# Optimization experiments

Hardware: AMD Instinct MI355X
Metric: run time of the kernel (lower is better)

Reference implementation:

```python
import jax, jax.numpy as jnp
import numpy as np

B, IC, H, W = 4, 512, 128, 128
INTER = IC // 32  # 16
C3 = 3 * INTER    # 48
EPS = 1e-5


def conv(x, w, b, pad, groups=1):
    y = jax.lax.conv_general_dilated(
        x, w, window_strides=(1, 1), padding=pad,
        dimension_numbers=('NCHW', 'OIHW', 'NCHW'),
        feature_group_count=groups)
    return y + b[None, :, None, None]


def bn(x, g, b, m, v):
    scale = (g * jax.lax.rsqrt(v + EPS))[None, :, None, None]
    return (x - m[None, :, None, None]) * scale + b[None, :, None, None]


def erode(x):
    # cv2.erode with ones(3,3): 3x3 sliding-window min, borders neutral (+inf)
    return jax.lax.reduce_window(x, jnp.array(jnp.inf, x.dtype), jax.lax.min,
                                 (1, 1, 3, 3), (1, 1, 1, 1), 'SAME')


def dilate(x):
    # cv2.dilate with ones(3,3): 3x3 sliding-window max, borders neutral (-inf)
    return jax.lax.reduce_window(x, jnp.array(-jnp.inf, x.dtype), jax.lax.max,
                                 (1, 1, 3, 3), (1, 1, 1, 1), 'SAME')


PH = [(1, 1), (0, 0)]  # (3,1)/(5,1) use vertical padding variants
PV = [(0, 0), (1, 1)]
PH5 = [(2, 2), (0, 0)]
PV5 = [(0, 0), (2, 2)]
P33 = [(1, 1), (1, 1)]


def gated_attention_fwd(ex, dx,
                        Dw1, Db1, Dw31, Db31, Dw13, Db13, Dw51, Db51, Dw15, Db15,
                        Dg, Dbe, Dm, Dv,
                        Ew1, Eb1, Ew31, Eb31, Ew13, Eb13, Ew51, Eb51, Ew15, Eb15,
                        Eg, Ebe, Em, Ev,
                        dww, dwb, pww, pwb,
                        qw, qb, kw, kb, vw, vb, rw, rb, cw, cb):
    b, c, h, w = ex.shape
    # ---- StripedConv subnetwork on dx ----
    dilX = dilate(dx)
    eroX = erode(dx)
    Dx1 = conv(dilX, Dw1, Db1, 'VALID')
    Dx31 = conv(dilX, Dw31, Db31, PH)
    Dx3113 = conv(Dx31, Dw13, Db13, PV)
    Dx51 = conv(dilX, Dw51, Db51, PH5)
    Dx5115 = conv(Dx51, Dw15, Db15, PV5)
    Ex1 = conv(eroX, Ew1, Eb1, 'VALID')
    Ex31 = conv(eroX, Ew31, Eb31, PH)
    Ex3113 = conv(Ex31, Ew13, Eb13, PV)
    Ex51 = conv(eroX, Ew51, Eb51, PH5)
    Ex5115 = conv(Ex51, Ew15, Eb15, PV5)
    difference = Dx1 - Ex51 + Dx1 - Ex31 + Dx31 - Ex1 + Dx51 - Ex1  # [b,16,h,w]
    dilF = jax.nn.relu(bn(jnp.concatenate([Dx1, Dx3113, Dx5115], axis=1), Dg, Dbe, Dm, Dv))
    eroF = jax.nn.relu(bn(jnp.concatenate([Ex1, Ex3113, Ex5115], axis=1), Eg, Ebe, Em, Ev))
    edge = jax.nn.relu(conv(conv(dilF - eroF, dww, dwb, P33, groups=C3), pww, pwb, 'VALID'))
    # ---- Gated attention on ex ----
    Q = conv(ex, qw, qb, 'VALID').reshape(b, INTER, -1)          # [b,16,hw]
    K = conv(ex, kw, kb, 'VALID').reshape(b, -1, INTER)          # reshape (NOT transpose), faithful to torch .view
    Wedge = jax.nn.sigmoid(conv(
        jnp.concatenate([jnp.mean(edge, axis=1, keepdims=True),
                         jnp.max(edge, axis=1, keepdims=True)], axis=1),
        cw, cb, 'VALID'))                                        # [b,1,h,w]
    V = conv(ex, vw, vb, 'VALID')
    V = (V * Wedge + V).reshape(b, INTER, -1)                    # [b,16,hw]
    diff = difference.reshape(b, -1, INTER)                      # [b,hw,16] via reshape
    weight = jnp.matmul(Q, K)                                    # [b,16,16]
    gate = jnp.matmul(Q, diff)                                   # [b,16,16]
    weights = jax.nn.softmax(weight + gate, axis=1)              # softmax over dim=1, per original
    atten = jnp.matmul(weights, V)                               # [b,16,hw]
    attenX = jnp.transpose(atten, (0, 2, 1)).reshape(b, INTER, h, w)
    out = conv(attenX, rw, rb, 'VALID') + dx                     # [b,512,h,w]
    return out


def setup_inputs() -> dict:
    key = jax.random.key(0)
    ks = iter(jax.random.split(key, 80))
    def rn(shape, s=0.05):
        return jax.random.normal(next(ks), shape, jnp.float32) * s
    inp = {}
    inp['ex'] = jax.random.normal(next(ks), (B, IC, H, W), jnp.float32)
    inp['dx'] = jax.random.normal(next(ks), (B, IC, H, W), jnp.float32)
    for p in ('D', 'E'):
        inp[p + 'w1'] = rn((INTER, IC, 1, 1)); inp[p + 'b1'] = rn((INTER,))
        inp[p + 'w31'] = rn((INTER, IC, 3, 1)); inp[p + 'b31'] = rn((INTER,))
        inp[p + 'w13'] = rn((INTER, INTER, 1, 3)); inp[p + 'b13'] = rn((INTER,))
        inp[p + 'w51'] = rn((INTER, IC, 5, 1)); inp[p + 'b51'] = rn((INTER,))
        inp[p + 'w15'] = rn((INTER, INTER, 1, 5)); inp[p + 'b15'] = rn((INTER,))
        inp[p + 'g'] = 1.0 + rn((C3,)); inp[p + 'be'] = rn((C3,))
        inp[p + 'm'] = rn((C3,), 0.1)
        inp[p + 'v'] = jax.random.uniform(next(ks), (C3,), jnp.float32, 0.5, 1.5)
    inp['dww'] = rn((C3, 1, 3, 3)); inp['dwb'] = rn((C3,))
    inp['pww'] = rn((INTER, C3, 1, 1)); inp['pwb'] = rn((INTER,))
    inp['qw'] = rn((INTER, IC, 1, 1)); inp['qb'] = rn((INTER,))
    inp['kw'] = rn((INTER, IC, 1, 1)); inp['kb'] = rn((INTER,))
    inp['vw'] = rn((INTER, IC, 1, 1)); inp['vb'] = rn((INTER,))
    inp['rw'] = rn((IC, INTER, 1, 1)); inp['rb'] = rn((IC,))
    inp['cw'] = rn((1, 2, 1, 1)); inp['cb'] = rn((1,))
    return inp


def reference(ex, dx,
              Dw1, Db1, Dw31, Db31, Dw13, Db13, Dw51, Db51, Dw15, Db15,
              Dg, Dbe, Dm, Dv,
              Ew1, Eb1, Ew31, Eb31, Ew13, Eb13, Ew51, Eb51, Ew15, Eb15,
              Eg, Ebe, Em, Ev,
              dww, dwb, pww, pwb,
              qw, qb, kw, kb, vw, vb, rw, rb, cw, cb):
    return gated_attention_fwd(ex, dx,
                               Dw1, Db1, Dw31, Db31, Dw13, Db13, Dw51, Db51, Dw15, Db15,
                               Dg, Dbe, Dm, Dv,
                               Ew1, Eb1, Ew31, Eb31, Ew13, Eb13, Ew51, Eb51, Ew15, Eb15,
                               Eg, Ebe, Em, Ev,
                               dww, dwb, pww, pwb,
                               qw, qb, kw, kb, vw, vb, rw, rb, cw, cb)
```

## Files before the change

### kernel.cpp

```cpp
#include <hip/hip_runtime.h>
#include <hip/hip_bf16.h>

typedef __hip_bfloat16 bf16_t;
typedef __attribute__((ext_vector_type(8))) short short8;
typedef __attribute__((ext_vector_type(4))) float floatx4;

constexpr int N_  = 4;
constexpr int C_  = 512;
constexpr int H_  = 128;
constexpr int W_  = 128;
constexpr int HW_ = H_ * W_;
constexpr int O144 = 144;
constexpr int C3_ = 48;

constexpr size_t OFF_DILT = 0;
constexpr size_t OFF_EROT = 67108864;
constexpr size_t OFF_PD   = 134217728;
constexpr size_t OFF_PE   = 171966464;
constexpr size_t OFF_WD   = 209715200;
constexpr size_t OFF_WE   = 210010112;
constexpr size_t OFF_WQ   = 210305024;
constexpr size_t OFF_BQ   = 210403328;
constexpr size_t OFF_WSUM = 210403584;
constexpr size_t OFF_WSM  = 210407680;
constexpr size_t OFF_DX1   = 0;
constexpr size_t OFF_DX31  = 4194304;
constexpr size_t OFF_DX51  = 8388608;
constexpr size_t OFF_EX1   = 12582912;
constexpr size_t OFF_EX31  = 16777216;
constexpr size_t OFF_EX51  = 20971520;
constexpr size_t OFF_DIFF  = 25165824;
constexpr size_t OFF_F     = 29360128;
constexpr size_t OFF_QKV   = 41943040;
constexpr size_t OFF_AX    = 54525952;
constexpr size_t OFF_WEDGE = 58720256;
constexpr size_t OFF_E16   = 67108864;

__global__ void prep_weights(const float* __restrict__ Dw1, const float* __restrict__ Dw31,
                             const float* __restrict__ Dw51,
                             const float* __restrict__ Ew1, const float* __restrict__ Ew31,
                             const float* __restrict__ Ew51,
                             const float* __restrict__ qw, const float* __restrict__ kw,
                             const float* __restrict__ vw,
                             const float* __restrict__ qb, const float* __restrict__ kb,
                             const float* __restrict__ vb,
                             bf16_t* __restrict__ WD, bf16_t* __restrict__ WE,
                             float* __restrict__ WQ, float* __restrict__ BQ) {
  int idx = blockIdx.x * 256 + threadIdx.x;
  const int sz = O144 * C_;
  if (idx < sz) {
    int r = idx / C_, c = idx % C_;
    float v;
    if (r < 16)       v = Dw1[r * C_ + c];
    else if (r < 64)  { int t = (r - 16) >> 4, o = (r - 16) & 15; v = Dw31[(o * C_ + c) * 3 + t]; }
    else              { int t = (r - 64) >> 4, o = (r - 64) & 15; v = Dw51[(o * C_ + c) * 5 + t]; }
    WD[idx] = __float2bfloat16(v);
    if (r < 16)       v = Ew1[r * C_ + c];
    else if (r < 64)  { int t = (r - 16) >> 4, o = (r - 16) & 15; v = Ew31[(o * C_ + c) * 3 + t]; }
    else              { int t = (r - 64) >> 4, o = (r - 64) & 15; v = Ew51[(o * C_ + c) * 5 + t]; }
    WE[idx] = __float2bfloat16(v);
  } else if (idx < sz + C3_ * C_) {
    int k = idx - sz;
    int r = k / C_, c = k % C_;
    const float* w = (r < 16) ? qw : (r < 32) ? kw : vw;
    WQ[k] = w[(r & 15) * C_ + c];
  } else if (idx < sz + C3_ * C_ + C3_) {
    int r = idx - sz - C3_ * C_;
    const float* bb = (r < 16) ? qb : (r < 32) ? kb : vb;
    BQ[r] = bb[r & 15];
  }
}

__device__ __forceinline__ void accrow(const float* __restrict__ rowp, int ax, int x0, int dx4,
                                       float* vmax, float* vmin) {
  float buf[16];
  *(float4*)&buf[0]  = *(const float4*)(rowp + ax);
  *(float4*)&buf[4]  = *(const float4*)(rowp + x0);
  *(float4*)&buf[8]  = *(const float4*)(rowp + x0 + 4);
  *(float4*)&buf[12] = *(const float4*)(rowp + dx4);
  #pragma unroll
  for (int j = 0; j < 10; ++j) {
    vmax[j] = fmaxf(vmax[j], buf[j + 3]);
    vmin[j] = fminf(vmin[j], buf[j + 3]);
  }
}

__global__ __launch_bounds__(256) void dilero_t(const float* __restrict__ dxin,
                                                bf16_t* __restrict__ dilT,
                                                bf16_t* __restrict__ eroT) {
  int cT = blockIdx.x, y = blockIdx.y, b = blockIdx.z;
  int t = threadIdx.x;
  int cl = t >> 4;
  int xg = t & 15, x0 = xg * 8;
  int c = cT * 16 + cl;
  const float* p = dxin + ((size_t)(b * C_ + c)) * HW_;
  int ax  = (x0 == 0)   ? 0   : x0 - 4;
  int dx4 = (x0 == 120) ? 124 : x0 + 8;
  float vmax[10], vmin[10];
  #pragma unroll
  for (int j = 0; j < 10; ++j) { vmax[j] = -INFINITY; vmin[j] = INFINITY; }
  if (y > 0)   accrow(p + (y - 1) * W_, ax, x0, dx4, vmax, vmin);
  accrow(p + y * W_, ax, x0, dx4, vmax, vmin);
  if (y < 127) accrow(p + (y + 1) * W_, ax, x0, dx4, vmax, vmin);
  if (xg == 0)  { vmax[0] = -INFINITY; vmin[0] = INFINITY; }
  if (xg == 15) { vmax[9] = -INFINITY; vmin[9] = INFINITY; }
  __shared__ bf16_t ds_d[128][18];
  __shared__ bf16_t ds_e[128][18];
  #pragma unroll
  for (int i = 0; i < 8; ++i) {
    float mx = fmaxf(fmaxf(vmax[i], vmax[i + 1]), vmax[i + 2]);
    float mn = fminf(fminf(vmin[i], vmin[i + 1]), vmin[i + 2]);
    ds_d[x0 + i][cl] = __float2bfloat16(mx);
    ds_e[x0 + i][cl] = __float2bfloat16(mn);
  }
  __syncthreads();
  int j = t & 127;
  const uint* rp = (t >> 7) ? (const uint*)&ds_e[j][0] : (const uint*)&ds_d[j][0];
  uint v0 = rp[0], v1 = rp[1], v2 = rp[2], v3 = rp[3];
  uint v4 = rp[4], v5 = rp[5], v6 = rp[6], v7 = rp[7];
  bf16_t* dst = (t >> 7) ? eroT : dilT;
  size_t base = ((size_t)(b * HW_ + y * W_ + j)) * C_ + cT * 16;
  uint4* op = (uint4*)(dst + base);
  op[0] = make_uint4(v0, v1, v2, v3);
  op[1] = make_uint4(v4, v5, v6, v7);
}

__global__ __launch_bounds__(256) void gemm_mfma(const bf16_t* __restrict__ WDb,
                                                 const bf16_t* __restrict__ WEb,
                                                 const bf16_t* __restrict__ DILt,
                                                 const bf16_t* __restrict__ EROt,
                                                 float* __restrict__ PD,
                                                 float* __restrict__ PE) {
  constexpr int LDA = 40;
  constexpr int LDB = 40;
  __shared__ bf16_t As[48 * LDA];
  __shared__ bf16_t Bs[128 * LDB];
  int z = blockIdx.z;
  int b = z & 3, map = z >> 2;
  const bf16_t* Wb = map ? WEb : WDb;
  const bf16_t* Xt = map ? EROt : DILt;
  float* Out = map ? PE : PD;
  int m0 = blockIdx.y * 48;
  int p0 = blockIdx.x * 128;
  int tid = threadIdx.x;
  int wave = tid >> 6, lane = tid & 63;
  int quad = lane >> 4, l16 = lane & 15;
  floatx4 acc[3][2] = {};
  const bf16_t* Xb = Xt + ((size_t)b * HW_ + p0) * C_;
  for (int k0 = 0; k0 < C_; k0 += 32) {
    if (tid < 192) {
      int m = tid >> 2, q = tid & 3;
      uint4 v = *(const uint4*)(Wb + (size_t)(m0 + m) * C_ + k0 + q * 8);
      *(uint4*)(&As[m * LDA + q * 8]) = v;
    }
    #pragma unroll
    for (int s = 0; s < 2; ++s) {
      int slot = tid + s * 256;
      int pp = slot >> 2, q = slot & 3;
      uint4 v = *(const uint4*)(Xb + (size_t)pp * C_ + k0 + q * 8);
      *(uint4*)(&Bs[pp * LDB + q * 8]) = v;
    }
    __syncthreads();
    short8 bfr[2];
    #pragma unroll
    for (int nt = 0; nt < 2; ++nt)
      bfr[nt] = *(const short8*)(&Bs[(wave * 32 + nt * 16 + l16) * LDB + quad * 8]);
    #pragma unroll
    for (int mt = 0; mt < 3; ++mt) {
      short8 afr = *(const short8*)(&As[(mt * 16 + l16) * LDA + quad * 8]);
      #pragma unroll
      for (int nt = 0; nt < 2; ++nt)
        acc[mt][nt] = __builtin_amdgcn_mfma_f32_16x16x32_bf16(afr, bfr[nt], acc[mt][nt], 0, 0, 0);
    }
    __syncthreads();
  }
  #pragma unroll
  for (int mt = 0; mt < 3; ++mt)
    #pragma unroll
    for (int nt = 0; nt < 2; ++nt) {
      int n = p0 + wave * 32 + nt * 16 + l16;
      #pragma unroll
      for (int r = 0; r < 4; ++r) {
        int m = m0 + mt * 16 + quad * 4 + r;
        Out[((size_t)b * O144 + m) * HW_ + n] = acc[mt][nt][r];
      }
    }
}

__global__ __launch_bounds__(256) void gemm48f(const float* __restrict__ X,
                                               const float* __restrict__ Wm,
                                               const float* __restrict__ bias,
                                               float* __restrict__ Out) {
  int b  = blockIdx.z;
  int p0 = blockIdx.x * 128;
  __shared__ __align__(16) float Xs[16][128];
  __shared__ __align__(16) float Ws[16][8][8];
  int tid = threadIdx.x;
  int pg  = tid & 31;
  int og  = tid >> 5;
  float acc[6][4] = {};
  const float* Xb = X + (size_t)b * C_ * HW_;
  for (int k0 = 0; k0 < C_; k0 += 16) {
    {
      int e = tid * 8;
      int kk = e >> 7, px = e & 127;
      float4 a = *(const float4*)(Xb + (size_t)(k0 + kk) * HW_ + p0 + px);
      float4 bv = *(const float4*)(Xb + (size_t)(k0 + kk) * HW_ + p0 + px + 4);
      *(float4*)&Xs[kk][px] = a;
      *(float4*)&Xs[kk][px + 4] = bv;
    }
    #pragma unroll
    for (int i = 0; i < 3; ++i) {
      int e = tid * 3 + i;
      int oo = e >> 4, kk = e & 15;
      Ws[kk][oo / 6][oo % 6] = Wm[(size_t)oo * C_ + k0 + kk];
    }
    __syncthreads();
    #pragma unroll
    for (int kk = 0; kk < 16; ++kk) {
      float4 xv = *(const float4*)&Xs[kk][pg * 4];
      float4 wa = *(const float4*)&Ws[kk][og][0];
      float2 wb = *(const float2*)&Ws[kk][og][4];
      float wv[6] = {wa.x, wa.y, wa.z, wa.w, wb.x, wb.y};
      float xs[4] = {xv.x, xv.y, xv.z, xv.w};
      #pragma unroll
      for (int o = 0; o < 6; ++o)
        #pragma unroll
        for (int pq = 0; pq < 4; ++pq) acc[o][pq] += wv[o] * xs[pq];
    }
    __syncthreads();
  }
  #pragma unroll
  for (int o = 0; o < 6; ++o) {
    int oc = og * 6 + o;
    float bi = bias[oc];
    float4 r;
    r.x = acc[o][0] + bi; r.y = acc[o][1] + bi; r.z = acc[o][2] + bi; r.w = acc[o][3] + bi;
    *(float4*)&Out[((size_t)b * C3_ + oc) * HW_ + p0 + pg * 4] = r;
  }
}

__global__ void combine(const float* __restrict__ PD, const float* __restrict__ PE,
                        const float* __restrict__ Db1, const float* __restrict__ Db31,
                        const float* __restrict__ Db51,
                        const float* __restrict__ Eb1, const float* __restrict__ Eb31,
                        const float* __restrict__ Eb51,
                        float* __restrict__ Dx1, float* __restrict__ Dx31, float* __restrict__ Dx51,
                        float* __restrict__ Ex1, float* __restrict__ Ex31, float* __restrict__ Ex51,
                        float* __restrict__ Diff) {
  int idx = blockIdx.x * 256 + threadIdx.x;
  int pix = idx & (HW_ - 1);
  int o = (idx >> 14) & 15;
  int b = idx >> 18;
  int y = pix >> 7;
  const float* pd = PD + (size_t)b * O144 * HW_;
  const float* pe = PE + (size_t)b * O144 * HW_;
  float d1 = pd[o * HW_ + pix] + Db1[o];
  float e1 = pe[o * HW_ + pix] + Eb1[o];
  float d31 = Db31[o], e31 = Eb31[o];
  #pragma unroll
  for (int t = 0; t < 3; ++t) {
    int yy = y - 1 + t;
    if (yy >= 0 && yy < H_) {
      int pp = pix + (t - 1) * W_;
      d31 += pd[(16 + t * 16 + o) * HW_ + pp];
      e31 += pe[(16 + t * 16 + o) * HW_ + pp];
    }
  }
  float d51 = Db51[o], e51 = Eb51[o];
  #pragma unroll
  for (int t = 0; t < 5; ++t) {
    int yy = y - 2 + t;
    if (yy >= 0 && yy < H_) {
      int pp = pix + (t - 2) * W_;
      d51 += pd[(64 + t * 16 + o) * HW_ + pp];
      e51 += pe[(64 + t * 16 + o) * HW_ + pp];
    }
  }
  Dx1[idx] = d1;  Ex1[idx] = e1;
  Dx31[idx] = d31; Ex31[idx] = e31;
  Dx51[idx] = d51; Ex51[idx] = e51;
  Diff[idx] = 2.f * d1 + d31 + d51 - 2.f * e1 - e31 - e51;
}

__device__ __forceinline__ void loadwin(const float* __restrict__ rowp, int xb, float* buf) {
  int a0 = (xb == 0)   ? 0   : xb - 4;
  int c0 = (xb == 124) ? 124 : xb + 4;
  *(float4*)&buf[0] = *(const float4*)(rowp + a0);
  *(float4*)&buf[4] = *(const float4*)(rowp + xb);
  *(float4*)&buf[8] = *(const float4*)(rowp + c0);
  if (xb == 0)   { buf[0] = buf[1] = buf[2] = buf[3] = 0.f; }
  if (xb == 124) { buf[8] = buf[9] = buf[10] = buf[11] = 0.f; }
}

__global__ __launch_bounds__(256) void fkern(const float* __restrict__ Dx1, const float* __restrict__ Dx31,
                      const float* __restrict__ Dx51,
                      const float* __restrict__ Ex1, const float* __restrict__ Ex31,
                      const float* __restrict__ Ex51,
                      const float* __restrict__ Dw13, const float* __restrict__ Db13,
                      const float* __restrict__ Dw15, const float* __restrict__ Db15,
                      const float* __restrict__ Ew13, const float* __restrict__ Eb13,
                      const float* __restrict__ Ew15, const float* __restrict__ Eb15,
                      const float* __restrict__ Dg, const float* __restrict__ Dbe,
                      const float* __restrict__ Dm, const float* __restrict__ Dv,
                      const float* __restrict__ Eg, const float* __restrict__ Ebe,
                      const float* __restrict__ Em, const float* __restrict__ Ev,
                      float* __restrict__ F) {
  int idx = blockIdx.x * 256 + threadIdx.x;
  int xq = idx & 4095;
  int ch = (idx >> 12) % 48;
  int b  = (idx >> 12) / 48;
  int pix4 = xq * 4;
  int xb = (xq & 31) * 4;
  int rowoff = pix4 - xb;
  float dval[4], eval[4];
  if (ch < 16) {
    const float* dp = Dx1 + (((size_t)(b * 16 + ch)) << 14) + pix4;
    const float* ep = Ex1 + (((size_t)(b * 16 + ch)) << 14) + pix4;
    float4 dv = *(const float4*)dp, ev = *(const float4*)ep;
    dval[0]=dv.x; dval[1]=dv.y; dval[2]=dv.z; dval[3]=dv.w;
    eval[0]=ev.x; eval[1]=ev.y; eval[2]=ev.z; eval[3]=ev.w;
  } else if (ch < 32) {
    int o = ch - 16;
    float da[4] = {Db13[o], Db13[o], Db13[o], Db13[o]};
    float ea[4] = {Eb13[o], Eb13[o], Eb13[o], Eb13[o]};
    for (int m = 0; m < 16; ++m) {
      float bd[12], be[12];
      loadwin(Dx31 + (((size_t)(b * 16 + m)) << 14) + rowoff, xb, bd);
      loadwin(Ex31 + (((size_t)(b * 16 + m)) << 14) + rowoff, xb, be);
      #pragma unroll
      for (int t = 0; t < 3; ++t) {
        float wd = Dw13[(o * 16 + m) * 3 + t];
        float we = Ew13[(o * 16 + m) * 3 + t];
        #pragma unroll
        for (int i = 0; i < 4; ++i) {
          da[i] += wd * bd[i + t + 3];
          ea[i] += we * be[i + t + 3];
        }
      }
    }
    #pragma unroll
    for (int i = 0; i < 4; ++i) { dval[i] = da[i]; eval[i] = ea[i]; }
  } else {
    int o = ch - 32;
    float da[4] = {Db15[o], Db15[o], Db15[o], Db15[o]};
    float ea[4] = {Eb15[o], Eb15[o], Eb15[o], Eb15[o]};
    for (int m = 0; m < 16; ++m) {
      float bd[12], be[12];
      loadwin(Dx51 + (((size_t)(b * 16 + m)) << 14) + rowoff, xb, bd);
      loadwin(Ex51 + (((size_t)(b * 16 + m)) << 14) + rowoff, xb, be);
      #pragma unroll
      for (int t = 0; t < 5; ++t) {
        float wd = Dw15[(o * 16 + m) * 5 + t];
        float we = Ew15[(o * 16 + m) * 5 + t];
        #pragma unroll
        for (int i = 0; i < 4; ++i) {
          da[i] += wd * bd[i + t + 2];
          ea[i] += we * be[i + t + 2];
        }
      }
    }
    #pragma unroll
    for (int i = 0; i < 4; ++i) { dval[i] = da[i]; eval[i] = ea[i]; }
  }
  float sD = Dg[ch] * rsqrtf(Dv[ch] + 1e-5f);
  float sE = Eg[ch] * rsqrtf(Ev[ch] + 1e-5f);
  float4 r;
  float* rr = (float*)&r;
  #pragma unroll
  for (int i = 0; i < 4; ++i) {
    float fD = fmaxf((dval[i] - Dm[ch]) * sD + Dbe[ch], 0.f);
    float fE = fmaxf((eval[i] - Em[ch]) * sE + Ebe[ch], 0.f);
    rr[i] = fD - fE;
  }
  *(float4*)&F[(((size_t)(b * 48 + ch)) << 14) + pix4] = r;
}

__global__ __launch_bounds__(256) void edgeA(const float* __restrict__ F, const float* __restrict__ dww,
                      const float* __restrict__ dwb, const float* __restrict__ pww,
                      const float* __restrict__ pwb, float* __restrict__ E16) {
  int idx = blockIdx.x * 256 + threadIdx.x;
  int xq = idx & 4095;
  int o  = (idx >> 12) & 15;
  int b  = idx >> 16;
  int pix4 = xq * 4;
  int xb = (xq & 31) * 4;
  int y  = pix4 >> 7;
  int rowoff = pix4 - xb - y * W_;
  const float* Fb = F + (((size_t)b * 48) << 14);
  float e[4] = {pwb[o], pwb[o], pwb[o], pwb[o]};
  for (int g = 0; g < 48; ++g) {
    float dw[4] = {dwb[g], dwb[g], dwb[g], dwb[g]};
    const float* plane = Fb + ((size_t)g << 14);
    #pragma unroll
    for (int dy = 0; dy < 3; ++dy) {
      int yy = y - 1 + dy;
      if (yy < 0 || yy >= H_) continue;
      float buf[12];
      loadwin(plane + yy * W_ + rowoff, xb, buf);
      #pragma unroll
      for (int t = 0; t < 3; ++t) {
        float w = dww[g * 9 + dy * 3 + t];
        #pragma unroll
        for (int i = 0; i < 4; ++i) dw[i] += w * buf[i + t + 3];
      }
    }
    float pw = pww[o * 48 + g];
    #pragma unroll
    for (int i = 0; i < 4; ++i) e[i] += pw * dw[i];
  }
  float4 r;
  r.x = fmaxf(e[0], 0.f); r.y = fmaxf(e[1], 0.f);
  r.z = fmaxf(e[2], 0.f); r.w = fmaxf(e[3], 0.f);
  *(float4*)&E16[(((size_t)(b * 16 + o)) << 14) + pix4] = r;
}

__global__ void edgeB(const float* __restrict__ E16, const float* __restrict__ cw,
                      const float* __restrict__ cb, float* __restrict__ Wedge) {
  int idx = blockIdx.x * 256 + threadIdx.x;
  int pix = idx & (HW_ - 1);
  int b = idx >> 14;
  float sum = 0.f, mx = -INFINITY;
  #pragma unroll
  for (int o = 0; o < 16; ++o) {
    float v = E16[(((size_t)(b * 16 + o)) << 14) + pix];
    sum += v; mx = fmaxf(mx, v);
  }
  float z = cw[0] * (sum * (1.f / 16.f)) + cw[1] * mx + cb[0];
  Wedge[idx] = 1.f / (1.f + expf(-z));
}

__global__ void attn_qk(const float* __restrict__ QKV, const float* __restrict__ Diff,
                        float* __restrict__ wsum) {
  int b = blockIdx.y;
  int i = threadIdx.x >> 4, j = threadIdx.x & 15;
  const float* Q  = QKV + (size_t)b * C3_ * HW_;
  const float* Kf = Q + 16 * HW_;
  const float* Df = Diff + (size_t)b * 16 * HW_;
  __shared__ float Qs[16][512];
  __shared__ float KD[512][16];
  float acc = 0.f;
  int p0 = blockIdx.x * 2048;
  for (int c0 = p0; c0 < p0 + 2048; c0 += 512) {
    for (int e = threadIdx.x; e < 16 * 512; e += 256) {
      int r = e >> 9, p = e & 511;
      Qs[r][p] = Q[(r << 14) + c0 + p];
    }
    for (int e = threadIdx.x; e < 512 * 16; e += 256) {
      int f = (c0 << 4) + e;
      KD[e >> 4][e & 15] = Kf[f] + Df[f];
    }
    __syncthreads();
    for (int p = 0; p < 512; ++p) acc += Qs[i][p] * KD[p][j];
    __syncthreads();
  }
  atomicAdd(&wsum[(b << 8) + threadIdx.x], acc);
}

__global__ void softmaxk(const float* __restrict__ wsum, float* __restrict__ wsm) {
  int b = blockIdx.x;
  __shared__ float s[16][16];
  __shared__ float colmx[16], colsum[16];
  int i = threadIdx.x >> 4, j = threadIdx.x & 15;
  s[i][j] = wsum[(b << 8) + threadIdx.x];
  __syncthreads();
  if (threadIdx.x < 16) {
    int jj = threadIdx.x;
    float mx = -INFINITY;
    for (int ii = 0; ii < 16; ++ii) mx = fmaxf(mx, s[ii][jj]);
    float sm = 0.f;
    for (int ii = 0; ii < 16; ++ii) sm += expf(s[ii][jj] - mx);
    colmx[jj] = mx; colsum[jj] = sm;
  }
  __syncthreads();
  wsm[(b << 8) + threadIdx.x] = expf(s[i][j] - colmx[j]) / colsum[j];
}

__global__ void attenx_k(const float* __restrict__ QKV, const float* __restrict__ wsm,
                         const float* __restrict__ Wedge, float* __restrict__ AX) {
  int idx = blockIdx.x * 256 + threadIdx.x;
  int pix = idx & (HW_ - 1);
  int m = (idx >> 14) & 15;
  int b = idx >> 18;
  __shared__ float ws[256];
  ws[threadIdx.x] = wsm[(b << 8) + threadIdx.x];
  __syncthreads();
  int q = (m << 10) + (pix >> 4);
  int r = pix & 15;
  const float* V = QKV + (size_t)b * C3_ * HW_ + (size_t)32 * HW_;
  float a = 0.f;
  #pragma unroll
  for (int s = 0; s < 16; ++s) a += ws[(r << 4) + s] * V[(s << 14) + q];
  AX[idx] = a * (1.f + Wedge[(b << 14) + q]);
}

__global__ __launch_bounds__(256) void finalconv(const float* __restrict__ AX,
                                                 const float* __restrict__ rw,
                                                 const float* __restrict__ rb,
                                                 const float* __restrict__ dxin,
                                                 float* __restrict__ out) {
  int blk = blockIdx.x;
  int b = blk >> 6;
  int p0 = (blk & 63) << 8;
  __shared__ float ax[16][256];
  for (int e = threadIdx.x; e < 16 * 256; e += 256) {
    int m = e >> 8, p = e & 255;
    ax[m][p] = AX[((size_t)(b * 16 + m) << 14) + p0 + p];
  }
  __syncthreads();
  int p = threadIdx.x;
  for (int oc = 0; oc < 512; ++oc) {
    float a = rb[oc];
    #pragma unroll
    for (int m = 0; m < 16; ++m) a += rw[oc * 16 + m] * ax[m][p];
    size_t oi = ((size_t)(b * C_ + oc) << 14) + p0 + p;
    out[oi] = a + dxin[oi];
  }
}

extern "C" void kernel_launch(void* const* d_in, const int* in_sizes, int n_in,
                              void* d_out, int out_size, void* d_ws, size_t ws_size,
                              hipStream_t stream) {
  (void)in_sizes; (void)n_in; (void)out_size; (void)ws_size;
  const float* ex   = (const float*)d_in[0];
  const float* dx   = (const float*)d_in[1];
  const float* Dw1  = (const float*)d_in[2];
  const float* Db1  = (const float*)d_in[3];
  const float* Dw31 = (const float*)d_in[4];
  const float* Db31 = (const float*)d_in[5];
  const float* Dw13 = (const float*)d_in[6];
  const float* Db13 = (const float*)d_in[7];
  const float* Dw51 = (const float*)d_in[8];
  const float* Db51 = (const float*)d_in[9];
  const float* Dw15 = (const float*)d_in[10];
  const float* Db15 = (const float*)d_in[11];
  const float* Dg   = (const float*)d_in[12];
  const float* Dbe  = (const float*)d_in[13];
  const float* Dm   = (const float*)d_in[14];
  const float* Dv   = (const float*)d_in[15];
  const float* Ew1  = (const float*)d_in[16];
  const float* Eb1  = (const float*)d_in[17];
  const float* Ew31 = (const float*)d_in[18];
  const float* Eb31 = (const float*)d_in[19];
  const float* Ew13 = (const float*)d_in[20];
  const float* Eb13 = (const float*)d_in[21];
  const float* Ew51 = (const float*)d_in[22];
  const float* Eb51 = (const float*)d_in[23];
  const float* Ew15 = (const float*)d_in[24];
  const float* Eb15 = (const float*)d_in[25];
  const float* Eg   = (const float*)d_in[26];
  const float* Ebe  = (const float*)d_in[27];
  const float* Em   = (const float*)d_in[28];
  const float* Ev   = (const float*)d_in[29];
  const float* dww  = (const float*)d_in[30];
  const float* dwb  = (const float*)d_in[31];
  const float* pww  = (const float*)d_in[32];
  const float* pwb  = (const float*)d_in[33];
  const float* qw   = (const float*)d_in[34];
  const float* qb   = (const float*)d_in[35];
  const float* kw   = (const float*)d_in[36];
  const float* kb   = (const float*)d_in[37];
  const float* vw   = (const float*)d_in[38];
  const float* vb   = (const float*)d_in[39];
  const float* rw   = (const float*)d_in[40];
  const float* rb   = (const float*)d_in[41];
  const float* cw   = (const float*)d_in[42];
  const float* cb   = (const float*)d_in[43];

  char* ws = (char*)d_ws;
  bf16_t* DILt = (bf16_t*)(ws + OFF_DILT);
  bf16_t* EROt = (bf16_t*)(ws + OFF_EROT);
  float* PD   = (float*)(ws + OFF_PD);
  float* PE   = (float*)(ws + OFF_PE);
  bf16_t* WDb = (bf16_t*)(ws + OFF_WD);
  bf16_t* WEb = (bf16_t*)(ws + OFF_WE);
  float* WQ   = (float*)(ws + OFF_WQ);
  float* BQ   = (float*)(ws + OFF_BQ);
  float* WSUM = (float*)(ws + OFF_WSUM);
  float* WSM  = (float*)(ws + OFF_WSM);
  float* DX1  = (float*)(ws + OFF_DX1);
  float* DX31 = (float*)(ws + OFF_DX31);
  float* DX51 = (float*)(ws + OFF_DX51);
  float* EX1  = (float*)(ws + OFF_EX1);
  float* EX31 = (float*)(ws + OFF_EX31);
  float* EX51 = (float*)(ws + OFF_EX51);
  float* DIFF = (float*)(ws + OFF_DIFF);
  float* Fb   = (float*)(ws + OFF_F);
  float* QKV  = (float*)(ws + OFF_QKV);
  float* AX   = (float*)(ws + OFF_AX);
  float* WEDG = (float*)(ws + OFF_WEDGE);
  float* E16  = (float*)(ws + OFF_E16);

  prep_weights<<<385, 256, 0, stream>>>(Dw1, Dw31, Dw51, Ew1, Ew31, Ew51,
                                        qw, kw, vw, qb, kb, vb, WDb, WEb, WQ, BQ);
  dilero_t<<<dim3(32, 128, 4), 256, 0, stream>>>(dx, DILt, EROt);
  gemm_mfma<<<dim3(128, 3, 8), 256, 0, stream>>>(WDb, WEb, DILt, EROt, PD, PE);
  combine<<<(N_ * 16 * HW_) / 256, 256, 0, stream>>>(PD, PE, Db1, Db31, Db51, Eb1, Eb31, Eb51,
                                                     DX1, DX31, DX51, EX1, EX31, EX51, DIFF);
  gemm48f<<<dim3(HW_ / 128, 1, N_), 256, 0, stream>>>(ex, WQ, BQ, QKV);
  fkern<<<(N_ * 48 * (HW_ / 4)) / 256, 256, 0, stream>>>(DX1, DX31, DX51, EX1, EX31, EX51,
                                                   Dw13, Db13, Dw15, Db15, Ew13, Eb13, Ew15, Eb15,
                                                   Dg, Dbe, Dm, Dv, Eg, Ebe, Em, Ev, Fb);
  edgeA<<<(N_ * 16 * (HW_ / 4)) / 256, 256, 0, stream>>>(Fb, dww, dwb, pww, pwb, E16);
  edgeB<<<(N_ * HW_) / 256, 256, 0, stream>>>(E16, cw, cb, WEDG);
  hipMemsetAsync(ws + OFF_WSUM, 0, 4096, stream);
  attn_qk<<<dim3(8, N_), 256, 0, stream>>>(QKV, DIFF, WSUM);
  softmaxk<<<N_, 256, 0, stream>>>(WSUM, WSM);
  attenx_k<<<(N_ * 16 * HW_) / 256, 256, 0, stream>>>(QKV, WSM, WEDG, AX);
  finalconv<<<(N_ * HW_) / 256, 256, 0, stream>>>(AX, rw, rb, dx, (float*)d_out);
}
```

Measured before the change: 919.7 us.

## Widen MFMA GEMM M-tile, split edge depthwise/pointwise, vectorize final conv

The bf16 MFMA GEMM now computes all 144 output rows per block instead of splitting them into three 48-row tiles, so each activation tile is loaded once rather than three times. The edge branch, which used to redo the 48-channel depthwise conv for each of 16 outputs, now runs the depthwise conv once into a buffer and a second kernel applies the pointwise conv, ReLU and gating. The final 1x1 conv uses float4 loads and stores, with each thread covering 32 output channels. The costs are more accumulator registers in the GEMM (lower occupancy, fewer blocks), an extra 48-channel intermediate buffer, and a 48-entry register array in edgeB2.

```diff
diff --git a/kernel.cpp b/kernel.cpp
--- a/kernel.cpp
+++ b/kernel.cpp
@@ -34,7 +34,7 @@
 constexpr size_t OFF_QKV   = 41943040;
 constexpr size_t OFF_AX    = 54525952;
 constexpr size_t OFF_WEDGE = 58720256;
-constexpr size_t OFF_E16   = 67108864;
+constexpr size_t OFF_DW    = 67108864;
 
 __global__ void prep_weights(const float* __restrict__ Dw1, const float* __restrict__ Dw31,
                              const float* __restrict__ Dw51,
@@ -133,32 +133,36 @@
                                                  float* __restrict__ PE) {
   constexpr int LDA = 40;
   constexpr int LDB = 40;
-  __shared__ bf16_t As[48 * LDA];
+  __shared__ bf16_t As[O144 * LDA];
   __shared__ bf16_t Bs[128 * LDB];
-  int z = blockIdx.z;
+  int z = blockIdx.y;
   int b = z & 3, map = z >> 2;
   const bf16_t* Wb = map ? WEb : WDb;
   const bf16_t* Xt = map ? EROt : DILt;
   float* Out = map ? PE : PD;
-  int m0 = blockIdx.y * 48;
   int p0 = blockIdx.x * 128;
   int tid = threadIdx.x;
   int wave = tid >> 6, lane = tid & 63;
   int quad = lane >> 4, l16 = lane & 15;
-  floatx4 acc[3][2] = {};
+  floatx4 acc[9][2] = {};
   const bf16_t* Xb = Xt + ((size_t)b * HW_ + p0) * C_;
   for (int k0 = 0; k0 < C_; k0 += 32) {
-    if (tid < 192) {
-      int m = tid >> 2, q = tid & 3;
-      uint4 v = *(const uint4*)(Wb + (size_t)(m0 + m) * C_ + k0 + q * 8);
-      *(uint4*)(&As[m * LDA + q * 8]) = v;
+    #pragma unroll
+    for (int s = 0; s < 2; ++s) {
+      int slot = tid + s * 256;
+      int m = slot >> 2, q = slot & 3;
+      *(uint4*)(&As[m * LDA + q * 8]) = *(const uint4*)(Wb + (size_t)m * C_ + k0 + q * 8);
+    }
+    if (tid < 64) {
+      int slot = tid + 512;
+      int m = slot >> 2, q = slot & 3;
+      *(uint4*)(&As[m * LDA + q * 8]) = *(const uint4*)(Wb + (size_t)m * C_ + k0 + q * 8);
     }
     #pragma unroll
     for (int s = 0; s < 2; ++s) {
       int slot = tid + s * 256;
       int pp = slot >> 2, q = slot & 3;
-      uint4 v = *(const uint4*)(Xb + (size_t)pp * C_ + k0 + q * 8);
-      *(uint4*)(&Bs[pp * LDB + q * 8]) = v;
+      *(uint4*)(&Bs[pp * LDB + q * 8]) = *(const uint4*)(Xb + (size_t)pp * C_ + k0 + q * 8);
     }
     __syncthreads();
     short8 bfr[2];
@@ -166,7 +170,7 @@
     for (int nt = 0; nt < 2; ++nt)
       bfr[nt] = *(const short8*)(&Bs[(wave * 32 + nt * 16 + l16) * LDB + quad * 8]);
     #pragma unroll
-    for (int mt = 0; mt < 3; ++mt) {
+    for (int mt = 0; mt < 9; ++mt) {
       short8 afr = *(const short8*)(&As[(mt * 16 + l16) * LDA + quad * 8]);
       #pragma unroll
       for (int nt = 0; nt < 2; ++nt)
@@ -175,13 +179,13 @@
     __syncthreads();
   }
   #pragma unroll
-  for (int mt = 0; mt < 3; ++mt)
+  for (int mt = 0; mt < 9; ++mt)
     #pragma unroll
     for (int nt = 0; nt < 2; ++nt) {
       int n = p0 + wave * 32 + nt * 16 + l16;
       #pragma unroll
       for (int r = 0; r < 4; ++r) {
-        int m = m0 + mt * 16 + quad * 4 + r;
+        int m = mt * 16 + quad * 4 + r;
         Out[((size_t)b * O144 + m) * HW_ + n] = acc[mt][nt][r];
       }
     }
@@ -376,55 +380,58 @@
   *(float4*)&F[(((size_t)(b * 48 + ch)) << 14) + pix4] = r;
 }
 
-__global__ __launch_bounds__(256) void edgeA(const float* __restrict__ F, const float* __restrict__ dww,
-                      const float* __restrict__ dwb, const float* __restrict__ pww,
-                      const float* __restrict__ pwb, float* __restrict__ E16) {
+__global__ __launch_bounds__(256) void edgeDW(const float* __restrict__ F,
+                                              const float* __restrict__ dww,
+                                              const float* __restrict__ dwb,
+                                              float* __restrict__ DW) {
   int idx = blockIdx.x * 256 + threadIdx.x;
   int xq = idx & 4095;
-  int o  = (idx >> 12) & 15;
-  int b  = idx >> 16;
+  int ch = (idx >> 12) % 48;
+  int b  = (idx >> 12) / 48;
   int pix4 = xq * 4;
   int xb = (xq & 31) * 4;
   int y  = pix4 >> 7;
-  int rowoff = pix4 - xb - y * W_;
-  const float* Fb = F + (((size_t)b * 48) << 14);
-  float e[4] = {pwb[o], pwb[o], pwb[o], pwb[o]};
-  for (int g = 0; g < 48; ++g) {
-    float dw[4] = {dwb[g], dwb[g], dwb[g], dwb[g]};
-    const float* plane = Fb + ((size_t)g << 14);
-    #pragma unroll
-    for (int dy = 0; dy < 3; ++dy) {
-      int yy = y - 1 + dy;
-      if (yy < 0 || yy >= H_) continue;
-      float buf[12];
-      loadwin(plane + yy * W_ + rowoff, xb, buf);
+  const float* plane = F + (((size_t)(b * 48 + ch)) << 14);
+  float acc[4];
+  float bi = dwb[ch];
+  acc[0] = bi; acc[1] = bi; acc[2] = bi; acc[3] = bi;
+  #pragma unroll
+  for (int dy = 0; dy < 3; ++dy) {
+    int yy = y - 1 + dy;
+    if (yy < 0 || yy >= H_) continue;
+    float buf[12];
+    loadwin(plane + yy * W_, xb, buf);
+    #pragma unroll
+    for (int t = 0; t < 3; ++t) {
+      float w = dww[ch * 9 + dy * 3 + t];
       #pragma unroll
-      for (int t = 0; t < 3; ++t) {
-        float w = dww[g * 9 + dy * 3 + t];
-        #pragma unroll
-        for (int i = 0; i < 4; ++i) dw[i] += w * buf[i + t + 3];
-      }
-    }
-    float pw = pww[o * 48 + g];
-    #pragma unroll
-    for (int i = 0; i < 4; ++i) e[i] += pw * dw[i];
-  }
-  float4 r;
-  r.x = fmaxf(e[0], 0.f); r.y = fmaxf(e[1], 0.f);
-  r.z = fmaxf(e[2], 0.f); r.w = fmaxf(e[3], 0.f);
-  *(float4*)&E16[(((size_t)(b * 16 + o)) << 14) + pix4] = r;
-}
-
-__global__ void edgeB(const float* __restrict__ E16, const float* __restrict__ cw,
-                      const float* __restrict__ cb, float* __restrict__ Wedge) {
+      for (int i = 0; i < 4; ++i) acc[i] += w * buf[i + t + 3];
+    }
+  }
+  float4 r; r.x = acc[0]; r.y = acc[1]; r.z = acc[2]; r.w = acc[3];
+  *(float4*)&DW[(((size_t)(b * 48 + ch)) << 14) + pix4] = r;
+}
+
+__global__ __launch_bounds__(256) void edgeB2(const float* __restrict__ DW,
+                                              const float* __restrict__ pww,
+                                              const float* __restrict__ pwb,
+                                              const float* __restrict__ cw,
+                                              const float* __restrict__ cb,
+                                              float* __restrict__ Wedge) {
   int idx = blockIdx.x * 256 + threadIdx.x;
   int pix = idx & (HW_ - 1);
   int b = idx >> 14;
+  float dwv[48];
+  #pragma unroll
+  for (int g = 0; g < 48; ++g)
+    dwv[g] = DW[(((size_t)(b * 48 + g)) << 14) + pix];
   float sum = 0.f, mx = -INFINITY;
-  #pragma unroll
   for (int o = 0; o < 16; ++o) {
-    float v = E16[(((size_t)(b * 16 + o)) << 14) + pix];
-    sum += v; mx = fmaxf(mx, v);
+    float e = pwb[o];
+    #pragma unroll
+    for (int g = 0; g < 48; ++g) e += pww[o * 48 + g] * dwv[g];
+    e = fmaxf(e, 0.f);
+    sum += e; mx = fmaxf(mx, e);
   }
   float z = cw[0] * (sum * (1.f / 16.f)) + cw[1] * mx + cb[0];
   Wedge[idx] = 1.f / (1.f + expf(-z));
@@ -494,27 +501,39 @@
   AX[idx] = a * (1.f + Wedge[(b << 14) + q]);
 }
 
-__global__ __launch_bounds__(256) void finalconv(const float* __restrict__ AX,
-                                                 const float* __restrict__ rw,
-                                                 const float* __restrict__ rb,
-                                                 const float* __restrict__ dxin,
-                                                 float* __restrict__ out) {
-  int blk = blockIdx.x;
-  int b = blk >> 6;
-  int p0 = (blk & 63) << 8;
-  __shared__ float ax[16][256];
-  for (int e = threadIdx.x; e < 16 * 256; e += 256) {
-    int m = e >> 8, p = e & 255;
-    ax[m][p] = AX[((size_t)(b * 16 + m) << 14) + p0 + p];
+__global__ __launch_bounds__(256) void finalconv2(const float* __restrict__ AX,
+                                                  const float* __restrict__ rw,
+                                                  const float* __restrict__ rb,
+                                                  const float* __restrict__ dxin,
+                                                  float* __restrict__ out) {
+  int p0 = blockIdx.x * 64;
+  int b  = blockIdx.y;
+  int t  = threadIdx.x;
+  __shared__ float ax[16][64];
+  {
+    int m = t >> 4, px = (t & 15) * 4;
+    *(float4*)&ax[m][px] = *(const float4*)&AX[((size_t)(b * 16 + m) << 14) + p0 + px];
   }
   __syncthreads();
-  int p = threadIdx.x;
-  for (int oc = 0; oc < 512; ++oc) {
-    float a = rb[oc];
-    #pragma unroll
-    for (int m = 0; m < 16; ++m) a += rw[oc * 16 + m] * ax[m][p];
-    size_t oi = ((size_t)(b * C_ + oc) << 14) + p0 + p;
-    out[oi] = a + dxin[oi];
+  int px4 = (t & 15) * 4;
+  int ocg = t >> 4;
+  float4 axr[16];
+  #pragma unroll
+  for (int m = 0; m < 16; ++m) axr[m] = *(const float4*)&ax[m][px4];
+  int oc0 = ocg * 32;
+  for (int oc = oc0; oc < oc0 + 32; ++oc) {
+    float bi = rb[oc];
+    float4 acc; acc.x = bi; acc.y = bi; acc.z = bi; acc.w = bi;
+    #pragma unroll
+    for (int m = 0; m < 16; ++m) {
+      float w = rw[oc * 16 + m];
+      acc.x += w * axr[m].x; acc.y += w * axr[m].y;
+      acc.z += w * axr[m].z; acc.w += w * axr[m].w;
+    }
+    size_t oi = ((size_t)(b * C_ + oc) << 14) + p0 + px4;
+    float4 dv = *(const float4*)&dxin[oi];
+    acc.x += dv.x; acc.y += dv.y; acc.z += dv.z; acc.w += dv.w;
+    *(float4*)&out[oi] = acc;
   }
 }
 
@@ -589,23 +608,23 @@
   float* QKV  = (float*)(ws + OFF_QKV);
   float* AX   = (float*)(ws + OFF_AX);
   float* WEDG = (float*)(ws + OFF_WEDGE);
-  float* E16  = (float*)(ws + OFF_E16);
+  float* DWb  = (float*)(ws + OFF_DW);
 
   prep_weights<<<385, 256, 0, stream>>>(Dw1, Dw31, Dw51, Ew1, Ew31, Ew51,
                                         qw, kw, vw, qb, kb, vb, WDb, WEb, WQ, BQ);
   dilero_t<<<dim3(32, 128, 4), 256, 0, stream>>>(dx, DILt, EROt);
-  gemm_mfma<<<dim3(128, 3, 8), 256, 0, stream>>>(WDb, WEb, DILt, EROt, PD, PE);
+  gemm_mfma<<<dim3(128, 8), 256, 0, stream>>>(WDb, WEb, DILt, EROt, PD, PE);
   combine<<<(N_ * 16 * HW_) / 256, 256, 0, stream>>>(PD, PE, Db1, Db31, Db51, Eb1, Eb31, Eb51,
                                                      DX1, DX31, DX51, EX1, EX31, EX51, DIFF);
   gemm48f<<<dim3(HW_ / 128, 1, N_), 256, 0, stream>>>(ex, WQ, BQ, QKV);
   fkern<<<(N_ * 48 * (HW_ / 4)) / 256, 256, 0, stream>>>(DX1, DX31, DX51, EX1, EX31, EX51,
                                                    Dw13, Db13, Dw15, Db15, Ew13, Eb13, Ew15, Eb15,
                                                    Dg, Dbe, Dm, Dv, Eg, Ebe, Em, Ev, Fb);
-  edgeA<<<(N_ * 16 * (HW_ / 4)) / 256, 256, 0, stream>>>(Fb, dww, dwb, pww, pwb, E16);
-  edgeB<<<(N_ * HW_) / 256, 256, 0, stream>>>(E16, cw, cb, WEDG);
+  edgeDW<<<(N_ * 48 * (HW_ / 4)) / 256, 256, 0, stream>>>(Fb, dww, dwb, DWb);
+  edgeB2<<<(N_ * HW_) / 256, 256, 0, stream>>>(DWb, pww, pwb, cw, cb, WEDG);
   hipMemsetAsync(ws + OFF_WSUM, 0, 4096, stream);
   attn_qk<<<dim3(8, N_), 256, 0, stream>>>(QKV, DIFF, WSUM);
   softmaxk<<<N_, 256, 0, stream>>>(WSUM, WSM);
   attenx_k<<<(N_ * 16 * HW_) / 256, 256, 0, stream>>>(QKV, WSM, WEDG, AX);
-  finalconv<<<(N_ * HW_) / 256, 256, 0, stream>>>(AX, rw, rb, dx, (float*)d_out);
-}
+  finalconv2<<<dim3(256, 4), 256, 0, stream>>>(AX, rw, rb, dx, (float*)d_out);
+}
```

Result: faster. 802.9 us (-12.7%).
